# Kernel optimization log

Measured on AMD Instinct MI355X. Metric: run time of the kernel, lower is better.

## Reference

```python
import jax, jax.numpy as jnp
import numpy as np
import math

DIM = 2048
N_HEADS = 32
N_KV_HEADS = 8
HEAD_DIM = DIM // N_HEADS  # 64
N_REP = N_HEADS // N_KV_HEADS  # 4
BSZ = 2
SEQLEN = 2048
ROPE_THETA = 10000.0


def setup_inputs() -> dict:
    key = jax.random.key(0)
    k_x, k_q, k_k, k_v, k_o = jax.random.split(key, 5)
    x = jax.random.normal(k_x, (BSZ, SEQLEN, DIM), dtype=jnp.float32)
    scale = 0.02
    wq = jax.random.normal(k_q, (N_HEADS * HEAD_DIM, DIM), dtype=jnp.float32) * scale
    wk = jax.random.normal(k_k, (N_KV_HEADS * HEAD_DIM, DIM), dtype=jnp.float32) * scale
    wv = jax.random.normal(k_v, (N_KV_HEADS * HEAD_DIM, DIM), dtype=jnp.float32) * scale
    wo = jax.random.normal(k_o, (DIM, N_HEADS * HEAD_DIM), dtype=jnp.float32) * scale
    # RoPE frequencies: freqs_cis = exp(i * t * theta^{-2j/d}), j in [0, d/2)
    inv_freq = 1.0 / (ROPE_THETA ** (np.arange(0, HEAD_DIM, 2, dtype=np.float32) / HEAD_DIM))
    t = np.arange(SEQLEN, dtype=np.float32)
    freqs = np.outer(t, inv_freq)  # [S, HEAD_DIM//2]
    freqs_cos = jnp.asarray(np.cos(freqs), dtype=jnp.float32)
    freqs_sin = jnp.asarray(np.sin(freqs), dtype=jnp.float32)
    # causal additive mask [1,1,S,S]
    neg_inf = jnp.finfo(jnp.float32).min
    mask = jnp.where(jnp.tril(jnp.ones((SEQLEN, SEQLEN), dtype=bool)), 0.0, neg_inf)
    mask = mask[None, None, :, :].astype(jnp.float32)
    return {"x": x, "freqs_cos": freqs_cos, "freqs_sin": freqs_sin, "mask": mask,
            "wq": wq, "wk": wk, "wv": wv, "wo": wo}


def _apply_rotary(xq, xk, cos, sin):
    # xq: [B,S,H,D], xk: [B,S,Hkv,D]; cos/sin: [S, D//2]
    def rot(t):
        tr = t.reshape(*t.shape[:-1], -1, 2)  # [..., D//2, 2]
        tr_r, tr_i = tr[..., 0], tr[..., 1]
        c = cos[None, :, None, :]
        s = sin[None, :, None, :]
        out_r = tr_r * c - tr_i * s
        out_i = tr_r * s + tr_i * c
        return jnp.stack([out_r, out_i], axis=-1).reshape(t.shape)
    return rot(xq), rot(xk)


def reference(x, freqs_cos, freqs_sin, mask, wq, wk, wv, wo):
    bsz, seqlen, _ = x.shape
    xq = jnp.einsum('bsd,ed->bse', x, wq).reshape(bsz, seqlen, N_HEADS, HEAD_DIM)
    xk = jnp.einsum('bsd,ed->bse', x, wk).reshape(bsz, seqlen, N_KV_HEADS, HEAD_DIM)
    xv = jnp.einsum('bsd,ed->bse', x, wv).reshape(bsz, seqlen, N_KV_HEADS, HEAD_DIM)
    xq, xk = _apply_rotary(xq, xk, freqs_cos, freqs_sin)
    # GQA: repeat_interleave kv heads
    xk = jnp.repeat(xk, N_REP, axis=2)  # [B,S,H,D]
    xv = jnp.repeat(xv, N_REP, axis=2)
    # [B,H,S,D]
    q = xq.transpose(0, 2, 1, 3)
    k = xk.transpose(0, 2, 1, 3)
    v = xv.transpose(0, 2, 1, 3)
    scores = jnp.einsum('bhqd,bhkd->bhqk', q, k) / math.sqrt(HEAD_DIM)
    scores = scores + mask
    probs = jax.nn.softmax(scores.astype(jnp.float32), axis=-1).astype(q.dtype)
    out = jnp.einsum('bhqk,bhkd->bhqd', probs, v)
    out = out.transpose(0, 2, 1, 3).reshape(bsz, seqlen, N_HEADS * HEAD_DIM)
    return jnp.einsum('bse,de->bsd', out, wo)
```

## Files before the change

kernel.cpp:

```cpp
#include <hip/hip_runtime.h>
#include <hip/hip_bf16.h>
#include <stdint.h>

typedef __bf16 bf16x8 __attribute__((ext_vector_type(8)));
typedef float f32x4 __attribute__((ext_vector_type(4)));
typedef unsigned short u16;
typedef u16 u16x8 __attribute__((ext_vector_type(8)));

__device__ __forceinline__ float bf2f(u16 u) {
  union { uint32_t i; float f; } v; v.i = uint32_t(u) << 16; return v.f;
}
__device__ __forceinline__ u16 f2bf(float f) {
  union { float f; uint32_t i; } v; v.f = f;
  uint32_t r = v.i + 0x7FFFu + ((v.i >> 16) & 1u);
  return (u16)(r >> 16);
}
__device__ __forceinline__ uint32_t pack2(float a, float b) {
  union { __bf16 h[2]; uint32_t u; } v;
  v.h[0] = (__bf16)a; v.h[1] = (__bf16)b; return v.u;
}
__device__ __forceinline__ float exp2x(float x) { return __builtin_amdgcn_exp2f(x); }

typedef __attribute__((address_space(1))) const uint32_t gas_u32;
typedef __attribute__((address_space(3))) uint32_t las_u32;
__device__ __forceinline__ void gload_lds16(const u16* g, u16* l) {
  __builtin_amdgcn_global_load_lds((gas_u32*)g, (las_u32*)l, 16, 0, 0);
}

__global__ __launch_bounds__(256) void conv4(
    const float* __restrict__ x, const float* __restrict__ wq,
    const float* __restrict__ wk, const float* __restrict__ wv,
    u16* __restrict__ Xb, u16* __restrict__ Wqb,
    u16* __restrict__ Wkb, u16* __restrict__ Wvb)
{
  int t = blockIdx.x * 256 + threadIdx.x;
  const float* src; u16* dst;
  if (t < 1048576)      { src = x;  dst = Xb; }
  else if (t < 1572864) { src = wq; dst = Wqb; t -= 1048576; }
  else if (t < 1703936) { src = wk; dst = Wkb; t -= 1572864; }
  else                  { src = wv; dst = Wvb; t -= 1703936; }
  const int i = t * 8;
  const float4 a = *reinterpret_cast<const float4*>(src + i);
  const float4 b = *reinterpret_cast<const float4*>(src + i + 4);
  u16x8 o;
  o[0] = f2bf(a.x); o[1] = f2bf(a.y); o[2] = f2bf(a.z); o[3] = f2bf(a.w);
  o[4] = f2bf(b.x); o[5] = f2bf(b.y); o[6] = f2bf(b.z); o[7] = f2bf(b.w);
  *reinterpret_cast<u16x8*>(dst + i) = o;
}

__global__ __launch_bounds__(256) void f32_to_bf16(
    const float* __restrict__ in, u16* __restrict__ out, int n)
{
  const int i = (blockIdx.x * 256 + threadIdx.x) * 8;
  if (i >= n) return;
  const float4 a = *reinterpret_cast<const float4*>(in + i);
  const float4 b = *reinterpret_cast<const float4*>(in + i + 4);
  u16x8 o;
  o[0] = f2bf(a.x); o[1] = f2bf(a.y); o[2] = f2bf(a.z); o[3] = f2bf(a.w);
  o[4] = f2bf(b.x); o[5] = f2bf(b.y); o[6] = f2bf(b.z); o[7] = f2bf(b.w);
  *reinterpret_cast<u16x8*>(out + i) = o;
}

__device__ __forceinline__ void gemm_core(
    const u16* __restrict__ A, const u16* __restrict__ Bw,
    int row0, int col0, int K,
    u16* As, u16* Bs, f32x4 acc[4][4])
{
  const int tid = threadIdx.x, wv = tid >> 6, lane = tid & 63;
  const int l15 = lane & 15, lhi = lane >> 4;
  const int wr = (wv >> 1) * 64, wc = (wv & 1) * 64;

  int srow[4], scol[4], ldso[4];
#pragma unroll
  for (int sh = 0; sh < 4; ++sh) {
    const int idx = sh * 256 + tid;
    srow[sh] = idx >> 3;
    scol[sh] = ((idx & 7) ^ (srow[sh] & 7)) * 8;
    ldso[sh] = (sh * 256 + wv * 64) * 8;
  }

  for (int k0 = 0; k0 < K; k0 += 64) {
#pragma unroll
    for (int sh = 0; sh < 4; ++sh)
      gload_lds16(A + (size_t)(row0 + srow[sh]) * K + k0 + scol[sh], As + ldso[sh]);
#pragma unroll
    for (int sh = 0; sh < 4; ++sh)
      gload_lds16(Bw + (size_t)(col0 + srow[sh]) * K + k0 + scol[sh], Bs + ldso[sh]);
    __syncthreads();

#pragma unroll
    for (int kc = 0; kc < 2; ++kc) {
      bf16x8 af[4], bfv[4];
#pragma unroll
      for (int i = 0; i < 4; ++i) {
        const int ra = wr + i * 16 + l15;
        af[i] = *reinterpret_cast<const bf16x8*>(
            reinterpret_cast<const char*>(As) +
            ((ra * 128 + kc * 64 + lhi * 16) ^ ((ra & 7) << 4)));
        const int rb = wc + i * 16 + l15;
        bfv[i] = *reinterpret_cast<const bf16x8*>(
            reinterpret_cast<const char*>(Bs) +
            ((rb * 128 + kc * 64 + lhi * 16) ^ ((rb & 7) << 4)));
      }
#pragma unroll
      for (int mi = 0; mi < 4; ++mi)
#pragma unroll
        for (int ni = 0; ni < 4; ++ni)
          acc[mi][ni] = __builtin_amdgcn_mfma_f32_16x16x32_bf16(af[mi], bfv[ni], acc[mi][ni], 0, 0, 0);
    }
    __syncthreads();
  }
}

template <int F32OUT, int TRANSC>
__global__ __launch_bounds__(256) void gemm_bt2(
    const u16* __restrict__ A, const u16* __restrict__ Bw, void* __restrict__ Cv,
    int N, int K, int ldc)
{
  __shared__ u16 As[128 * 64];
  __shared__ u16 Bs[128 * 64];
  const int row0 = blockIdx.y * 128, col0 = blockIdx.x * 128;
  f32x4 acc[4][4] = {};
  gemm_core(A, Bw, row0, col0, K, As, Bs, acc);

  const int lane = threadIdx.x & 63, wv = threadIdx.x >> 6;
  const int wr = (wv >> 1) * 64, wc = (wv & 1) * 64;
  const int l15 = lane & 15;
#pragma unroll
  for (int mi = 0; mi < 4; ++mi) {
    const int r0 = row0 + wr + mi * 16 + ((lane >> 4) << 2);
#pragma unroll
    for (int ni = 0; ni < 4; ++ni) {
      const int c = col0 + wc + ni * 16 + l15;
#pragma unroll
      for (int r = 0; r < 4; ++r) {
        if (TRANSC)
          reinterpret_cast<u16*>(Cv)[(size_t)c * ldc + (r0 + r)] = f2bf(acc[mi][ni][r]);
        else if (F32OUT)
          reinterpret_cast<float*>(Cv)[(size_t)(r0 + r) * ldc + c] = acc[mi][ni][r];
        else
          reinterpret_cast<u16*>(Cv)[(size_t)(r0 + r) * ldc + c] = f2bf(acc[mi][ni][r]);
      }
    }
  }
}

__global__ __launch_bounds__(256) void gemm_kv(
    const u16* __restrict__ A, const u16* __restrict__ Wk, const u16* __restrict__ Wv,
    u16* __restrict__ Kout, u16* __restrict__ VTout, int K)
{
  __shared__ u16 As[128 * 64];
  __shared__ u16 Bs[128 * 64];
  const bool isV = blockIdx.x >= 4;
  const int col0 = (blockIdx.x & 3) * 128;
  const int row0 = blockIdx.y * 128;
  f32x4 acc[4][4] = {};
  gemm_core(A, isV ? Wv : Wk, row0, col0, K, As, Bs, acc);

  const int lane = threadIdx.x & 63, wv = threadIdx.x >> 6;
  const int wr = (wv >> 1) * 64, wc = (wv & 1) * 64;
  const int l15 = lane & 15;
#pragma unroll
  for (int mi = 0; mi < 4; ++mi) {
    const int r0 = row0 + wr + mi * 16 + ((lane >> 4) << 2);
#pragma unroll
    for (int ni = 0; ni < 4; ++ni) {
      const int c = col0 + wc + ni * 16 + l15;
#pragma unroll
      for (int r = 0; r < 4; ++r) {
        if (isV)
          VTout[(size_t)c * 4096 + (r0 + r)] = f2bf(acc[mi][ni][r]);
        else
          Kout[(size_t)(r0 + r) * 512 + c] = f2bf(acc[mi][ni][r]);
      }
    }
  }
}

__global__ __launch_bounds__(256) void rope_kernel(
    u16* __restrict__ Q, u16* __restrict__ Kv,
    const float* __restrict__ cosb, const float* __restrict__ sinb)
{
  const int QV = 4096 * 2048 / 8;
  const int KV = 4096 * 512 / 8;
  int t = blockIdx.x * 256 + threadIdx.x;
  u16* ptr; int shift; float scl;
  if (t < QV) { ptr = Q; shift = 11; scl = 0.125f * 1.44269504088896f; }
  else { t -= QV; if (t >= KV) return; ptr = Kv; shift = 9; scl = 1.f; }
  const int e = t * 8;
  const int row = e >> shift;
  const int col = e & ((1 << shift) - 1);
  const int s = row & 2047;
  const int j0 = (col & 63) >> 1;
  u16* p = ptr + ((size_t)row << shift) + col;
  u16x8 x = *reinterpret_cast<const u16x8*>(p);
  const float4 cv = *reinterpret_cast<const float4*>(cosb + s * 32 + j0);
  const float4 sv = *reinterpret_cast<const float4*>(sinb + s * 32 + j0);
  const float cf[4] = {cv.x, cv.y, cv.z, cv.w};
  const float sf[4] = {sv.x, sv.y, sv.z, sv.w};
  u16x8 o;
#pragma unroll
  for (int q = 0; q < 4; ++q) {
    const float xr = bf2f(x[2 * q]), xi = bf2f(x[2 * q + 1]);
    o[2 * q]     = f2bf((xr * cf[q] - xi * sf[q]) * scl);
    o[2 * q + 1] = f2bf((xr * sf[q] + xi * cf[q]) * scl);
  }
  *reinterpret_cast<u16x8*>(p) = o;
}

__device__ __forceinline__ bf16x8 lds_read8(const u16* base, int row, int col) {
  const int byte = (row * 128 + col * 2) ^ ((row & 7) << 4);
  return *reinterpret_cast<const bf16x8*>(reinterpret_cast<const char*>(base) + byte);
}
__device__ __forceinline__ void lds_write4(u16* base, int row, int col, uint32_t v) {
  const int byte = (row * 128 + col * 2) ^ ((row & 7) << 4);
  *reinterpret_cast<uint32_t*>(reinterpret_cast<char*>(base) + byte) = v;
}

__device__ __forceinline__ void attn_set(
    const u16* __restrict__ Ks, const u16* __restrict__ Vt, u16* __restrict__ Plw,
    const bf16x8 qf[2], int t0, int qbase, int l15, int lhi,
    float& mrun, float& lrun, f32x4 oacc[4])
{
  f32x4 s[4] = {};
#pragma unroll
  for (int kc = 0; kc < 2; ++kc)
#pragma unroll
    for (int f = 0; f < 4; ++f) {
      const bf16x8 kf = lds_read8(Ks, f * 16 + l15, kc * 32 + lhi * 8);
      s[f] = __builtin_amdgcn_mfma_f32_16x16x32_bf16(kf, qf[kc], s[f], 0, 0, 0);
    }
  const bool needmask = (t0 + 63 > qbase);
  float v[4][4];
  float mx = -1e30f;
#pragma unroll
  for (int f = 0; f < 4; ++f)
#pragma unroll
    for (int r = 0; r < 4; ++r) {
      float x = s[f][r];
      if (needmask && (t0 + f * 16 + lhi * 4 + r > qbase + l15)) x = -1e30f;
      v[f][r] = x;
      mx = fmaxf(mx, x);
    }
  mx = fmaxf(mx, __shfl_xor(mx, 16));
  mx = fmaxf(mx, __shfl_xor(mx, 32));
  if (!__all(mx <= mrun + 8.f)) {
    const float newm = fmaxf(mrun, mx);
    const float fac = exp2x(mrun - newm);
    mrun = newm;
    lrun *= fac;
    float facq[4];
#pragma unroll
    for (int r = 0; r < 4; ++r) facq[r] = __shfl(fac, lhi * 4 + r);
#pragma unroll
    for (int nf = 0; nf < 4; ++nf)
#pragma unroll
      for (int r = 0; r < 4; ++r) oacc[nf][r] *= facq[r];
  }
  float sum = 0.f;
#pragma unroll
  for (int f = 0; f < 4; ++f) {
    const float p0 = exp2x(v[f][0] - mrun), p1 = exp2x(v[f][1] - mrun);
    const float p2 = exp2x(v[f][2] - mrun), p3 = exp2x(v[f][3] - mrun);
    sum += (p0 + p1) + (p2 + p3);
    lds_write4(Plw, l15, f * 16 + lhi * 4,     pack2(p0, p1));
    lds_write4(Plw, l15, f * 16 + lhi * 4 + 2, pack2(p2, p3));
  }
  sum += __shfl_xor(sum, 16);
  sum += __shfl_xor(sum, 32);
  lrun += sum;
#pragma unroll
  for (int kc = 0; kc < 2; ++kc) {
    const bf16x8 pa = lds_read8(Plw, l15, kc * 32 + lhi * 8);
#pragma unroll
    for (int nf = 0; nf < 4; ++nf) {
      const bf16x8 vf = lds_read8(Vt, nf * 16 + l15, kc * 32 + lhi * 8);
      oacc[nf] = __builtin_amdgcn_mfma_f32_16x16x32_bf16(pa, vf, oacc[nf], 0, 0, 0);
    }
  }
}

__device__ __forceinline__ void attn_store(
    u16* __restrict__ O, const size_t qoff, const int h, const int qbase,
    const int l15, const int lhi, const float lrun, const f32x4 oacc[4])
{
  float linv[4];
#pragma unroll
  for (int r = 0; r < 4; ++r) linv[r] = 1.f / __shfl(lrun, lhi * 4 + r);
#pragma unroll
  for (int nf = 0; nf < 4; ++nf)
#pragma unroll
    for (int r = 0; r < 4; ++r)
      O[qoff + (size_t)(qbase + lhi * 4 + r) * 2048 + h * 64 + nf * 16 + l15] =
          f2bf(oacc[nf][r] * linv[r]);
}

__global__ __launch_bounds__(256) void attn_kernel(
    const u16* __restrict__ Q, const u16* __restrict__ K,
    const u16* __restrict__ VT, u16* __restrict__ O)
{
  __shared__ u16 Ks[2][64 * 64];
  __shared__ u16 Vt[2][64 * 64];
  __shared__ u16 Pl[4][16 * 64];

  const int j  = blockIdx.x;
  const int h  = blockIdx.y;
  const int b  = blockIdx.z;
  const int kh = h >> 2;
  const int tid = threadIdx.x, wv = tid >> 6, lane = tid & 63;
  const int l15 = lane & 15, lhi = lane >> 4;
  const size_t qoff = (size_t)b * 2048 * 2048;
  const size_t koff = (size_t)b * 2048 * 512;

  const int qAb = j * 64 + wv * 16;
  const int qBb = (31 - j) * 64 + wv * 16;

  const int idx0 = tid, idx1 = tid + 256;
  const int r0 = idx0 >> 3, u0 = (idx0 & 7) ^ (r0 & 7);
  const int r1 = idx1 >> 3, u1 = (idx1 & 7) ^ (r1 & 7);
  const u16* const kg0 = K + koff + (size_t)r0 * 512 + kh * 64 + u0 * 8;
  const u16* const kg1 = K + koff + (size_t)r1 * 512 + kh * 64 + u1 * 8;
  const u16* const vg0 = VT + (size_t)(kh * 64 + r0) * 4096 + b * 2048 + u0 * 8;
  const u16* const vg1 = VT + (size_t)(kh * 64 + r1) * 4096 + b * 2048 + u1 * 8;
  const int ld0 = wv * 512;
  const int ld1 = 2048 + wv * 512;

  bf16x8 qfA[2], qfB[2];
#pragma unroll
  for (int kc = 0; kc < 2; ++kc) {
    qfA[kc] = *reinterpret_cast<const bf16x8*>(
        Q + qoff + (size_t)(qAb + l15) * 2048 + h * 64 + kc * 32 + lhi * 8);
    qfB[kc] = *reinterpret_cast<const bf16x8*>(
        Q + qoff + (size_t)(qBb + l15) * 2048 + h * 64 + kc * 32 + lhi * 8);
  }

  float mA = -1e30f, lA = 0.f, mB = -1e30f, lB = 0.f;
  f32x4 oA[4] = {}, oB[4] = {};

  const int tlast = 31 - j;

  gload_lds16(kg0, &Ks[0][ld0]);
  gload_lds16(kg1, &Ks[0][ld1]);
  gload_lds16(vg0, &Vt[0][ld0]);
  gload_lds16(vg1, &Vt[0][ld1]);
  __syncthreads();

  int cur = 0;
  for (int t = 0; t <= tlast; ++t) {
    const int t0 = t * 64;
    if (t < tlast) {
      const int n0 = t0 + 64;
      const int nb = cur ^ 1;
      gload_lds16(kg0 + (size_t)n0 * 512, &Ks[nb][ld0]);
      gload_lds16(kg1 + (size_t)n0 * 512, &Ks[nb][ld1]);
      gload_lds16(vg0 + n0, &Vt[nb][ld0]);
      gload_lds16(vg1 + n0, &Vt[nb][ld1]);
    }

    if (t <= j)
      attn_set(Ks[cur], Vt[cur], Pl[wv], qfA, t0, qAb, l15, lhi, mA, lA, oA);
    attn_set(Ks[cur], Vt[cur], Pl[wv], qfB, t0, qBb, l15, lhi, mB, lB, oB);

    __syncthreads();
    cur ^= 1;
  }

  attn_store(O, qoff, h, qAb, l15, lhi, lA, oA);
  attn_store(O, qoff, h, qBb, l15, lhi, lB, oB);
}

extern "C" void kernel_launch(void* const* d_in, const int* in_sizes, int n_in,
                              void* d_out, int out_size, void* d_ws, size_t ws_size,
                              hipStream_t stream)
{
  const float* x  = (const float*)d_in[0];
  const float* fc = (const float*)d_in[1];
  const float* fs = (const float*)d_in[2];
  const float* wq = (const float*)d_in[4];
  const float* wk = (const float*)d_in[5];
  const float* wv = (const float*)d_in[6];
  const float* wo = (const float*)d_in[7];
  float* out = (float*)d_out;

  u16* Xb  = (u16*)d_ws;
  u16* Wqb = Xb  + (size_t)4096 * 2048;
  u16* Wkb = Wqb + (size_t)2048 * 2048;
  u16* Wvb = Wkb + (size_t)512 * 2048;
  u16* Qws = Wvb + (size_t)512 * 2048;
  u16* Kws = Qws + (size_t)4096 * 2048;
  u16* VTws = Kws + (size_t)4096 * 512;
  u16* Ows = Xb;
  u16* Wob = Wqb;

  dim3 blk(256);
  conv4<<<dim3((1048576 + 524288 + 131072 + 131072) / 256), blk, 0, stream>>>(
      x, wq, wk, wv, Xb, Wqb, Wkb, Wvb);
  gemm_bt2<0,0><<<dim3(16, 32), blk, 0, stream>>>(Xb, Wqb, Qws, 2048, 2048, 2048);
  gemm_kv<<<dim3(8, 32), blk, 0, stream>>>(Xb, Wkb, Wvb, Kws, VTws, 2048);
  f32_to_bf16<<<dim3(2048 * 2048 / 8 / 256), blk, 0, stream>>>(wo, Wob, 2048 * 2048);
  rope_kernel<<<dim3((4096 * 2048 / 8 + 4096 * 512 / 8) / 256), blk, 0, stream>>>(Qws, Kws, fc, fs);
  attn_kernel<<<dim3(16, 32, 2), blk, 0, stream>>>(Qws, Kws, VTws, Ows);
  gemm_bt2<1,0><<<dim3(16, 32), blk, 0, stream>>>(Ows, Wob, out, 2048, 2048, 2048);
}
```

Measured before the change: 277.2 us.

## Compute softmax row sums via MFMA with ones, swizzle GEMM block order

```diff
diff --git a/kernel.cpp b/kernel.cpp
--- a/kernel.cpp
+++ b/kernel.cpp
@@ -20,6 +20,9 @@
   v.h[0] = (__bf16)a; v.h[1] = (__bf16)b; return v.u;
 }
 __device__ __forceinline__ float exp2x(float x) { return __builtin_amdgcn_exp2f(x); }
+__device__ __forceinline__ float max3f(float a, float b, float c) {
+  return fmaxf(fmaxf(a, b), c);
+}
 
 typedef __attribute__((address_space(1))) const uint32_t gas_u32;
 typedef __attribute__((address_space(3))) uint32_t las_u32;
@@ -119,7 +122,10 @@
 {
   __shared__ u16 As[128 * 64];
   __shared__ u16 Bs[128 * 64];
-  const int row0 = blockIdx.y * 128, col0 = blockIdx.x * 128;
+  const int nwg = gridDim.x * gridDim.y;
+  int lin = blockIdx.y * gridDim.x + blockIdx.x;
+  lin = (lin & 7) * (nwg >> 3) + (lin >> 3);
+  const int row0 = (lin / gridDim.x) * 128, col0 = (lin % gridDim.x) * 128;
   f32x4 acc[4][4] = {};
   gemm_core(A, Bw, row0, col0, K, As, Bs, acc);
 
@@ -151,9 +157,12 @@
 {
   __shared__ u16 As[128 * 64];
   __shared__ u16 Bs[128 * 64];
-  const bool isV = blockIdx.x >= 4;
-  const int col0 = (blockIdx.x & 3) * 128;
-  const int row0 = blockIdx.y * 128;
+  int lin = blockIdx.y * 8 + blockIdx.x;
+  lin = (lin & 7) * 32 + (lin >> 3);
+  const int bx = lin & 7, by = lin >> 3;
+  const bool isV = bx >= 4;
+  const int col0 = (bx & 3) * 128;
+  const int row0 = by * 128;
   f32x4 acc[4][4] = {};
   gemm_core(A, isV ? Wv : Wk, row0, col0, K, As, Bs, acc);
 
@@ -219,8 +228,8 @@
 
 __device__ __forceinline__ void attn_set(
     const u16* __restrict__ Ks, const u16* __restrict__ Vt, u16* __restrict__ Plw,
-    const bf16x8 qf[2], int t0, int qbase, int l15, int lhi,
-    float& mrun, float& lrun, f32x4 oacc[4])
+    const bf16x8 qf[2], const bf16x8 ones, int t0, int qbase, int l15, int lhi,
+    float& mrun, f32x4& lrun, f32x4 oacc[4])
 {
   f32x4 s[4] = {};
 #pragma unroll
@@ -232,7 +241,6 @@
     }
   const bool needmask = (t0 + 63 > qbase);
   float v[4][4];
-  float mx = -1e30f;
 #pragma unroll
   for (int f = 0; f < 4; ++f)
 #pragma unroll
@@ -240,38 +248,40 @@
       float x = s[f][r];
       if (needmask && (t0 + f * 16 + lhi * 4 + r > qbase + l15)) x = -1e30f;
       v[f][r] = x;
-      mx = fmaxf(mx, x);
-    }
+    }
+  float t1 = max3f(v[0][0], v[0][1], v[0][2]);
+  float t2 = max3f(v[0][3], v[1][0], v[1][1]);
+  float t3 = max3f(v[1][2], v[1][3], v[2][0]);
+  float t4 = max3f(v[2][1], v[2][2], v[2][3]);
+  float t5 = max3f(v[3][0], v[3][1], v[3][2]);
+  float mx = fmaxf(max3f(t1, t2, t3), max3f(t4, t5, v[3][3]));
   mx = fmaxf(mx, __shfl_xor(mx, 16));
   mx = fmaxf(mx, __shfl_xor(mx, 32));
   if (!__all(mx <= mrun + 8.f)) {
     const float newm = fmaxf(mrun, mx);
     const float fac = exp2x(mrun - newm);
     mrun = newm;
-    lrun *= fac;
     float facq[4];
 #pragma unroll
     for (int r = 0; r < 4; ++r) facq[r] = __shfl(fac, lhi * 4 + r);
 #pragma unroll
+    for (int r = 0; r < 4; ++r) lrun[r] *= facq[r];
+#pragma unroll
     for (int nf = 0; nf < 4; ++nf)
 #pragma unroll
       for (int r = 0; r < 4; ++r) oacc[nf][r] *= facq[r];
   }
-  float sum = 0.f;
 #pragma unroll
   for (int f = 0; f < 4; ++f) {
     const float p0 = exp2x(v[f][0] - mrun), p1 = exp2x(v[f][1] - mrun);
     const float p2 = exp2x(v[f][2] - mrun), p3 = exp2x(v[f][3] - mrun);
-    sum += (p0 + p1) + (p2 + p3);
     lds_write4(Plw, l15, f * 16 + lhi * 4,     pack2(p0, p1));
     lds_write4(Plw, l15, f * 16 + lhi * 4 + 2, pack2(p2, p3));
   }
-  sum += __shfl_xor(sum, 16);
-  sum += __shfl_xor(sum, 32);
-  lrun += sum;
 #pragma unroll
   for (int kc = 0; kc < 2; ++kc) {
     const bf16x8 pa = lds_read8(Plw, l15, kc * 32 + lhi * 8);
+    lrun = __builtin_amdgcn_mfma_f32_16x16x32_bf16(pa, ones, lrun, 0, 0, 0);
 #pragma unroll
     for (int nf = 0; nf < 4; ++nf) {
       const bf16x8 vf = lds_read8(Vt, nf * 16 + l15, kc * 32 + lhi * 8);
@@ -282,11 +292,11 @@
 
 __device__ __forceinline__ void attn_store(
     u16* __restrict__ O, const size_t qoff, const int h, const int qbase,
-    const int l15, const int lhi, const float lrun, const f32x4 oacc[4])
+    const int l15, const int lhi, const f32x4 lrun, const f32x4 oacc[4])
 {
   float linv[4];
 #pragma unroll
-  for (int r = 0; r < 4; ++r) linv[r] = 1.f / __shfl(lrun, lhi * 4 + r);
+  for (int r = 0; r < 4; ++r) linv[r] = 1.f / lrun[r];
 #pragma unroll
   for (int nf = 0; nf < 4; ++nf)
 #pragma unroll
@@ -333,8 +343,12 @@
     qfB[kc] = *reinterpret_cast<const bf16x8*>(
         Q + qoff + (size_t)(qBb + l15) * 2048 + h * 64 + kc * 32 + lhi * 8);
   }
-
-  float mA = -1e30f, lA = 0.f, mB = -1e30f, lB = 0.f;
+  bf16x8 ones;
+#pragma unroll
+  for (int i = 0; i < 8; ++i) ones[i] = (__bf16)1.0f;
+
+  float mA = -1e30f, mB = -1e30f;
+  f32x4 lA = {}, lB = {};
   f32x4 oA[4] = {}, oB[4] = {};
 
   const int tlast = 31 - j;
@@ -358,8 +372,8 @@
     }
 
     if (t <= j)
-      attn_set(Ks[cur], Vt[cur], Pl[wv], qfA, t0, qAb, l15, lhi, mA, lA, oA);
-    attn_set(Ks[cur], Vt[cur], Pl[wv], qfB, t0, qBb, l15, lhi, mB, lB, oB);
+      attn_set(Ks[cur], Vt[cur], Pl[wv], qfA, ones, t0, qAb, l15, lhi, mA, lA, oA);
+    attn_set(Ks[cur], Vt[cur], Pl[wv], qfB, ones, t0, qBb, l15, lhi, mB, lB, oB);
 
     __syncthreads();
     cur ^= 1;
```

Result: no change. 272.4 us (-1.7%).
